# Kernel optimization log

Hardware: AMD Instinct MI355X
Metric: run time of the kernel (lower is better)

## Reference

```python
import jax, jax.numpy as jnp
import numpy as np

BSZ, MAX_LEN, INPUT_DIM = 4, 256, 1024
BIAFFINE, OUT, N_HEAD = 512, 512, 4
IN_HD = BIAFFINE // N_HEAD   # 128
OUT_HD = OUT // N_HEAD       # 128


def setup_inputs() -> dict:
    key = jax.random.key(0)
    ks = jax.random.split(key, 6)
    x = jax.random.normal(ks[0], (BSZ, MAX_LEN, INPUT_DIM), dtype=jnp.float32)
    # head/tail MLP linear params (dropout is identity at inference)
    scale_lin = 1.0 / np.sqrt(INPUT_DIM)
    Wh = jax.random.normal(ks[1], (BIAFFINE, INPUT_DIM), dtype=jnp.float32) * scale_lin
    bh = jnp.zeros((BIAFFINE,), dtype=jnp.float32)
    Wv = jax.random.normal(ks[2], (BIAFFINE, INPUT_DIM), dtype=jnp.float32) * scale_lin
    bv = jnp.zeros((BIAFFINE,), dtype=jnp.float32)
    # biaffine tensor, xavier_normal over last two dims fan
    xav = np.sqrt(2.0 / (IN_HD + IN_HD))
    W = jax.random.normal(ks[3], (N_HEAD, OUT_HD, IN_HD, IN_HD), dtype=jnp.float32) * xav
    return {"x": x, "Wh": Wh, "bh": bh, "Wv": Wv, "bv": bv, "W": W}


def reference(x, Wh, bh, Wv, bv, W):
    # head/tail MLPs: Linear + LeakyReLU (slope 0.01, torch default)
    h = jax.nn.leaky_relu(jnp.einsum('bld,od->blo', x, Wh) + bh)  # b l biaffine
    v = jax.nn.leaky_relu(jnp.einsum('bld,od->blo', x, Wv) + bv)
    bsz, max_len, _ = h.shape
    h = h.reshape(bsz, max_len, N_HEAD, IN_HD)
    v = v.reshape(bsz, max_len, N_HEAD, IN_HD)
    # 3-way biaffine contraction
    w = jnp.einsum('blhx,hdxy,bkhy->bhdlk', h, W, v)  # b h out_hd l k
    w = w.reshape(bsz, OUT, max_len, max_len)
    return jnp.transpose(w, (0, 2, 3, 1))  # b l k out
```

## Files before the change

### kernel.cpp

```cpp
#include <hip/hip_runtime.h>


typedef unsigned short u16;
typedef __attribute__((ext_vector_type(8))) short short8;
typedef __attribute__((ext_vector_type(4))) float f32x4;

typedef __attribute__((address_space(1))) const unsigned gu32;
typedef __attribute__((address_space(3))) unsigned lu32;

__device__ __forceinline__ u16 f2bf(float f) {
  union { float f; unsigned u; } c; c.f = f;
  unsigned u = c.u;
  return (u16)((u + 0x7FFFu + ((u >> 16) & 1u)) >> 16);
}

__device__ __forceinline__ unsigned pack2(float a, float b) {
  return ((unsigned)f2bf(b) << 16) | (unsigned)f2bf(a);
}

__device__ __forceinline__ uint4 pack8(const float* __restrict__ g) {
  float4 f0 = *(const float4*)(g);
  float4 f1 = *(const float4*)(g + 4);
  uint4 o;
  o.x = pack2(f0.x, f0.y);
  o.y = pack2(f0.z, f0.w);
  o.z = pack2(f1.x, f1.y);
  o.w = pack2(f1.z, f1.w);
  return o;
}

__device__ __forceinline__ void tile_compute(const u16* As, const u16* Bs,
                                             f32x4 acc[4][4], int wm, int wn,
                                             int frow, int kq) {
  short8 af[4], bfr[4];
#pragma unroll
  for (int i = 0; i < 4; ++i)
    af[i] = *(const short8*)(As + (size_t)(wm + i * 16 + frow) * 32 + kq);
#pragma unroll
  for (int j = 0; j < 4; ++j)
    bfr[j] = *(const short8*)(Bs + (size_t)(wn + j * 16 + frow) * 32 + kq);
#pragma unroll
  for (int i = 0; i < 4; ++i)
#pragma unroll
    for (int j = 0; j < 4; ++j)
      acc[i][j] = __builtin_amdgcn_mfma_f32_16x16x32_bf16(af[i], bfr[j], acc[i][j], 0, 0, 0);
}

__device__ __forceinline__ void stage_tile(const u16* __restrict__ g,
                                           u16* lds, int wave, int lane) {
#pragma unroll
  for (int t = 0; t < 8; ++t) {
    int qb = wave * 512 + t * 64;
    int q = qb + lane;
    const u16* src = g + (size_t)((q & 127) * 128 + (q >> 7) * 8);
    __builtin_amdgcn_global_load_lds((gu32*)src, (lu32*)(lds + (size_t)qb * 8),
                                     16, 0, 0);
  }
}

__device__ __forceinline__ void compute_fullK(const u16* As, const u16* Bs,
                                              f32x4 acc[4][4], int wm, int wn,
                                              int frow, int chi) {
#pragma unroll
  for (int ks = 0; ks < 4; ++ks) {
    int c = ks * 4 + chi;
    short8 af[4], bfr[4];
#pragma unroll
    for (int i = 0; i < 4; ++i)
      af[i] = *(const short8*)(As + ((size_t)c * 128 + wm + i * 16 + frow) * 8);
#pragma unroll
    for (int j = 0; j < 4; ++j)
      bfr[j] = *(const short8*)(Bs + ((size_t)c * 128 + wn + j * 16 + frow) * 8);
#pragma unroll
    for (int i = 0; i < 4; ++i)
#pragma unroll
      for (int j = 0; j < 4; ++j)
        acc[i][j] = __builtin_amdgcn_mfma_f32_16x16x32_bf16(af[i], bfr[j], acc[i][j], 0, 0, 0);
  }
}

__global__ __launch_bounds__(256) void k0_twp(const float* __restrict__ W,
                                              u16* __restrict__ Wb) {
  __shared__ u16 t[128][129];
  int slice = blockIdx.x;
  const float* src = W + (size_t)slice * 16384;
  u16* dst = Wb + (size_t)slice * 16384;
  int tid = threadIdx.x;
  for (int e = tid; e < 16384; e += 256) {
    int xi = e >> 7, yi = e & 127;
    t[xi][yi] = f2bf(src[e]);
  }
  __syncthreads();
  for (int e = tid; e < 16384; e += 256) {
    int yi = e >> 7, xi = e & 127;
    dst[e] = t[xi][yi];
  }
}

__global__ __launch_bounds__(256) void k1_mlp(const float* __restrict__ x,
                                              const float* __restrict__ Wh,
                                              const float* __restrict__ bh,
                                              const float* __restrict__ Wv,
                                              const float* __restrict__ bv,
                                              u16* __restrict__ hmat,
                                              u16* __restrict__ vmat) {
  __shared__ __align__(16) u16 As[128 * 32];
  __shared__ __align__(16) u16 Bs[128 * 32];
  int tid = threadIdx.x;
  int m0 = blockIdx.y * 128;
  int n0 = blockIdx.x * 128;
  bool isV = (n0 >= 512);
  const float* Wsel = isV ? Wv : Wh;
  const float* bsel = isV ? bv : bh;
  int nW = isV ? (n0 - 512) : n0;
  int wave = tid >> 6, lane = tid & 63;
  int wm = (wave & 1) * 64, wn = (wave >> 1) * 64;
  int r = tid >> 1, seg = tid & 1;
  int frow = lane & 15, kq = (lane >> 4) * 8;
  f32x4 acc[4][4];
  f32x4 z = {0.f, 0.f, 0.f, 0.f};
#pragma unroll
  for (int i = 0; i < 4; ++i)
#pragma unroll
    for (int j = 0; j < 4; ++j) acc[i][j] = z;

  for (int k0 = 0; k0 < 1024; k0 += 32) {
    const float* ga = x + (size_t)(m0 + r) * 1024 + k0 + seg * 16;
    const float* gb = Wsel + (size_t)(nW + r) * 1024 + k0 + seg * 16;
    uint4 a0 = pack8(ga), a1 = pack8(ga + 8);
    uint4 b0 = pack8(gb), b1 = pack8(gb + 8);
    __syncthreads();
    *(uint4*)(As + r * 32 + seg * 16) = a0;
    *(uint4*)(As + r * 32 + seg * 16 + 8) = a1;
    *(uint4*)(Bs + r * 32 + seg * 16) = b0;
    *(uint4*)(Bs + r * 32 + seg * 16 + 8) = b1;
    __syncthreads();
    tile_compute(As, Bs, acc, wm, wn, frow, kq);
  }

  u16* dst = isV ? vmat : hmat;
#pragma unroll
  for (int i = 0; i < 4; ++i)
#pragma unroll
    for (int j = 0; j < 4; ++j)
#pragma unroll
      for (int rg = 0; rg < 4; ++rg) {
        int ml = wm + i * 16 + (lane >> 4) * 4 + rg;
        int nl = wn + j * 16 + (lane & 15);
        int mg = m0 + ml;
        int ng = n0 + nl;
        float val = acc[i][j][rg] + bsel[nW + nl];
        val = (val >= 0.f) ? val : 0.01f * val;
        int bb = mg >> 8, ll = mg & 255;
        int head = (ng & 511) >> 7, xcol = ng & 127;
        dst[(((size_t)(bb * 4 + head)) * 256 + ll) * 128 + xcol] = f2bf(val);
      }
}

__global__ __launch_bounds__(256) void k2_uw(const u16* __restrict__ hmat,
                                             const u16* __restrict__ Wb,
                                             u16* __restrict__ u, int b0) {
  __shared__ __align__(16) u16 As[16384];
  __shared__ __align__(16) u16 Bs[16384];
  int tid = threadIdx.x, wave = tid >> 6, lane = tid & 63;
  int z = blockIdx.z;
  int b = b0 + (z >> 2), h = z & 3;
  int n0 = blockIdx.x * 128;
  int m0 = blockIdx.y * 128;
  const u16* A = hmat + ((size_t)(b * 4 + h) * 256 + m0) * 128;
  const u16* Bt = Wb + ((size_t)h * 16384 + n0) * 128;
  stage_tile(A, As, wave, lane);
  stage_tile(Bt, Bs, wave, lane);

  int wm = (wave & 1) * 64, wn = (wave >> 1) * 64;
  int frow = lane & 15, chi = lane >> 4;
  f32x4 acc[4][4];
  f32x4 zz = {0.f, 0.f, 0.f, 0.f};
#pragma unroll
  for (int i = 0; i < 4; ++i)
#pragma unroll
    for (int j = 0; j < 4; ++j) acc[i][j] = zz;

  __syncthreads();
  compute_fullK(As, Bs, acc, wm, wn, frow, chi);

  u16* C = u + ((size_t)z * 256 + m0) * 16384 + n0;
#pragma unroll
  for (int i = 0; i < 4; ++i)
#pragma unroll
    for (int j = 0; j < 4; ++j)
#pragma unroll
      for (int rg = 0; rg < 4; ++rg) {
        int ml = wm + i * 16 + (lane >> 4) * 4 + rg;
        int nl = wn + j * 16 + (lane & 15);
        C[(size_t)ml * 16384 + nl] = f2bf(acc[i][j][rg]);
      }
}

__global__ __launch_bounds__(256) void k3_out(const u16* __restrict__ vmat,
                                              const u16* __restrict__ u,
                                              float* __restrict__ out, int b0) {
  __shared__ __align__(16) u16 As[16384];
  __shared__ __align__(16) u16 Bs[16384];
  int tid = threadIdx.x, wave = tid >> 6, lane = tid & 63;
  int z = blockIdx.z;
  int b = b0 + (z >> 2), h = z & 3;
  int l = blockIdx.x;
  int k0t = blockIdx.y * 128;
  const u16* A = vmat + ((size_t)(b * 4 + h) * 256 + k0t) * 128;
  const u16* Bt = u + ((size_t)z * 256 + l) * 16384;
  stage_tile(A, As, wave, lane);
  stage_tile(Bt, Bs, wave, lane);

  int wm = (wave & 1) * 64, wn = (wave >> 1) * 64;
  int frow = lane & 15, chi = lane >> 4;
  f32x4 acc[4][4];
  f32x4 zz = {0.f, 0.f, 0.f, 0.f};
#pragma unroll
  for (int i = 0; i < 4; ++i)
#pragma unroll
    for (int j = 0; j < 4; ++j) acc[i][j] = zz;

  __syncthreads();
  compute_fullK(As, Bs, acc, wm, wn, frow, chi);

#pragma unroll
  for (int i = 0; i < 4; ++i)
#pragma unroll
    for (int j = 0; j < 4; ++j)
#pragma unroll
      for (int rg = 0; rg < 4; ++rg) {
        int kk = k0t + wm + i * 16 + (lane >> 4) * 4 + rg;
        int d = wn + j * 16 + (lane & 15);
        out[(((size_t)b * 256 + l) * 256 + kk) * 512 + h * 128 + d] = acc[i][j][rg];
      }
}

extern "C" void kernel_launch(void* const* d_in, const int* in_sizes, int n_in,
                              void* d_out, int out_size, void* d_ws, size_t ws_size,
                              hipStream_t stream) {
  const float* x = (const float*)d_in[0];
  const float* Wh = (const float*)d_in[1];
  const float* bh = (const float*)d_in[2];
  const float* Wv = (const float*)d_in[3];
  const float* bv = (const float*)d_in[4];
  const float* W = (const float*)d_in[5];
  float* out = (float*)d_out;

  char* ws = (char*)d_ws;
  u16* Wb = (u16*)(ws);
  u16* hmat = (u16*)(ws + (16u << 20));
  u16* vmat = (u16*)(ws + (17u << 20));
  u16* u = (u16*)(ws + (18u << 20));

  hipLaunchKernelGGL(k0_twp, dim3(512), dim3(256), 0, stream, W, Wb);
  hipLaunchKernelGGL(k1_mlp, dim3(8, 8), dim3(256), 0, stream, x, Wh, bh, Wv, bv,
                     hmat, vmat);

  size_t need = (18ull << 20) + (128ull << 20);
  if (ws_size >= need) {
    hipLaunchKernelGGL(k2_uw, dim3(128, 2, 16), dim3(256), 0, stream, hmat, Wb, u, 0);
    hipLaunchKernelGGL(k3_out, dim3(256, 2, 16), dim3(256), 0, stream, vmat, u, out, 0);
  } else {
    for (int b = 0; b < 4; ++b) {
      hipLaunchKernelGGL(k2_uw, dim3(128, 2, 4), dim3(256), 0, stream, hmat, Wb, u, b);
      hipLaunchKernelGGL(k3_out, dim3(256, 2, 4), dim3(256), 0, stream, vmat, u, out, b);
    }
  }
}
```

Measured before the change: 727.7 us.

## Pre-tile operands in chunked layout for contiguous LDS staging and XOR-swizzled u loads

The h/v projections and the transposed biaffine weight are now written in a k-chunked tile layout, so each 128x128 tile is one contiguous 32KB block. The block can then be staged into LDS with linear global_load_lds instead of the strided gather used before. The u operand in k3 is staged with an XOR swizzle on the chunk index, and the fragment reads apply the matching swizzle, which is meant to coalesce global reads of u rows and avoid LDS bank conflicts. The blockIdx.z mapping is reordered to put head outermost, which changes how blocks are grouped when they run.

```diff
diff --git a/kernel.cpp b/kernel.cpp
--- a/kernel.cpp
+++ b/kernel.cpp
@@ -29,38 +29,32 @@
   return o;
 }
 
-__device__ __forceinline__ void tile_compute(const u16* As, const u16* Bs,
-                                             f32x4 acc[4][4], int wm, int wn,
-                                             int frow, int kq) {
-  short8 af[4], bfr[4];
-#pragma unroll
-  for (int i = 0; i < 4; ++i)
-    af[i] = *(const short8*)(As + (size_t)(wm + i * 16 + frow) * 32 + kq);
-#pragma unroll
-  for (int j = 0; j < 4; ++j)
-    bfr[j] = *(const short8*)(Bs + (size_t)(wn + j * 16 + frow) * 32 + kq);
-#pragma unroll
-  for (int i = 0; i < 4; ++i)
-#pragma unroll
-    for (int j = 0; j < 4; ++j)
-      acc[i][j] = __builtin_amdgcn_mfma_f32_16x16x32_bf16(af[i], bfr[j], acc[i][j], 0, 0, 0);
-}
-
-__device__ __forceinline__ void stage_tile(const u16* __restrict__ g,
-                                           u16* lds, int wave, int lane) {
+__device__ __forceinline__ void stage_linear(const u16* __restrict__ g,
+                                             u16* lds, int wave, int lane) {
+#pragma unroll
+  for (int t = 0; t < 8; ++t) {
+    int qb = wave * 512 + t * 64;
+    __builtin_amdgcn_global_load_lds((gu32*)(g + (size_t)(qb + lane) * 8),
+                                     (lu32*)(lds + (size_t)qb * 8), 16, 0, 0);
+  }
+}
+
+__device__ __forceinline__ void stage_xor(const u16* __restrict__ g,
+                                          u16* lds, int wave, int lane) {
 #pragma unroll
   for (int t = 0; t < 8; ++t) {
     int qb = wave * 512 + t * 64;
     int q = qb + lane;
-    const u16* src = g + (size_t)((q & 127) * 128 + (q >> 7) * 8);
-    __builtin_amdgcn_global_load_lds((gu32*)src, (lu32*)(lds + (size_t)qb * 8),
-                                     16, 0, 0);
-  }
-}
-
-__device__ __forceinline__ void compute_fullK(const u16* As, const u16* Bs,
-                                              f32x4 acc[4][4], int wm, int wn,
-                                              int frow, int chi) {
+    int row = q >> 4, c = q & 15;
+    int su = row * 16 + (c ^ (row & 7));
+    __builtin_amdgcn_global_load_lds((gu32*)(g + (size_t)su * 8),
+                                     (lu32*)(lds + (size_t)qb * 8), 16, 0, 0);
+  }
+}
+
+__device__ __forceinline__ void compute_kk(const u16* As, const u16* Bs,
+                                           f32x4 acc[4][4], int wm, int wn,
+                                           int frow, int chi) {
 #pragma unroll
   for (int ks = 0; ks < 4; ++ks) {
     int c = ks * 4 + chi;
@@ -71,6 +65,29 @@
 #pragma unroll
     for (int j = 0; j < 4; ++j)
       bfr[j] = *(const short8*)(Bs + ((size_t)c * 128 + wn + j * 16 + frow) * 8);
+#pragma unroll
+    for (int i = 0; i < 4; ++i)
+#pragma unroll
+      for (int j = 0; j < 4; ++j)
+        acc[i][j] = __builtin_amdgcn_mfma_f32_16x16x32_bf16(af[i], bfr[j], acc[i][j], 0, 0, 0);
+  }
+}
+
+__device__ __forceinline__ void compute_kx(const u16* As, const u16* Bs,
+                                           f32x4 acc[4][4], int wm, int wn,
+                                           int frow, int chi) {
+#pragma unroll
+  for (int ks = 0; ks < 4; ++ks) {
+    int c = ks * 4 + chi;
+    short8 af[4], bfr[4];
+#pragma unroll
+    for (int i = 0; i < 4; ++i)
+      af[i] = *(const short8*)(As + ((size_t)c * 128 + wm + i * 16 + frow) * 8);
+#pragma unroll
+    for (int j = 0; j < 4; ++j) {
+      int rn = wn + j * 16 + frow;
+      bfr[j] = *(const short8*)(Bs + ((size_t)rn * 16 + (c ^ (rn & 7))) * 8);
+    }
 #pragma unroll
     for (int i = 0; i < 4; ++i)
 #pragma unroll
@@ -92,8 +109,8 @@
   }
   __syncthreads();
   for (int e = tid; e < 16384; e += 256) {
-    int yi = e >> 7, xi = e & 127;
-    dst[e] = t[xi][yi];
+    int c = e >> 10, rem = e & 1023, y = rem >> 3, xl = rem & 7;
+    dst[e] = t[c * 8 + xl][y];
   }
 }
 
@@ -135,7 +152,18 @@
     *(uint4*)(Bs + r * 32 + seg * 16) = b0;
     *(uint4*)(Bs + r * 32 + seg * 16 + 8) = b1;
     __syncthreads();
-    tile_compute(As, Bs, acc, wm, wn, frow, kq);
+    short8 af[4], bfr[4];
+#pragma unroll
+    for (int i = 0; i < 4; ++i)
+      af[i] = *(const short8*)(As + (size_t)(wm + i * 16 + frow) * 32 + kq);
+#pragma unroll
+    for (int j = 0; j < 4; ++j)
+      bfr[j] = *(const short8*)(Bs + (size_t)(wn + j * 16 + frow) * 32 + kq);
+#pragma unroll
+    for (int i = 0; i < 4; ++i)
+#pragma unroll
+      for (int j = 0; j < 4; ++j)
+        acc[i][j] = __builtin_amdgcn_mfma_f32_16x16x32_bf16(af[i], bfr[j], acc[i][j], 0, 0, 0);
   }
 
   u16* dst = isV ? vmat : hmat;
@@ -152,39 +180,42 @@
         float val = acc[i][j][rg] + bsel[nW + nl];
         val = (val >= 0.f) ? val : 0.01f * val;
         int bb = mg >> 8, ll = mg & 255;
-        int head = (ng & 511) >> 7, xcol = ng & 127;
-        dst[(((size_t)(bb * 4 + head)) * 256 + ll) * 128 + xcol] = f2bf(val);
+        int head = (ng & 511) >> 7, xc = ng & 127;
+        int zi = head * 4 + bb;
+        dst[((size_t)zi * 2 + (ll >> 7)) * 16384 + (xc >> 3) * 1024 +
+            (ll & 127) * 8 + (xc & 7)] = f2bf(val);
       }
 }
 
 __global__ __launch_bounds__(256) void k2_uw(const u16* __restrict__ hmat,
                                              const u16* __restrict__ Wb,
-                                             u16* __restrict__ u, int b0) {
+                                             u16* __restrict__ u, int b0, int nz) {
   __shared__ __align__(16) u16 As[16384];
   __shared__ __align__(16) u16 Bs[16384];
   int tid = threadIdx.x, wave = tid >> 6, lane = tid & 63;
-  int z = blockIdx.z;
-  int b = b0 + (z >> 2), h = z & 3;
-  int n0 = blockIdx.x * 128;
+  int zz = blockIdx.z;
+  int h, b;
+  if (nz == 16) { h = zz >> 2; b = zz & 3; } else { h = zz; b = b0; }
+  int zi_hm = h * 4 + b;
+  int zi_u = zz;
+  int d = blockIdx.x;
   int m0 = blockIdx.y * 128;
-  const u16* A = hmat + ((size_t)(b * 4 + h) * 256 + m0) * 128;
-  const u16* Bt = Wb + ((size_t)h * 16384 + n0) * 128;
-  stage_tile(A, As, wave, lane);
-  stage_tile(Bt, Bs, wave, lane);
+  stage_linear(hmat + ((size_t)zi_hm * 2 + (m0 >> 7)) * 16384, As, wave, lane);
+  stage_linear(Wb + ((size_t)h * 128 + d) * 16384, Bs, wave, lane);
 
   int wm = (wave & 1) * 64, wn = (wave >> 1) * 64;
   int frow = lane & 15, chi = lane >> 4;
   f32x4 acc[4][4];
-  f32x4 zz = {0.f, 0.f, 0.f, 0.f};
-#pragma unroll
-  for (int i = 0; i < 4; ++i)
-#pragma unroll
-    for (int j = 0; j < 4; ++j) acc[i][j] = zz;
+  f32x4 zz4 = {0.f, 0.f, 0.f, 0.f};
+#pragma unroll
+  for (int i = 0; i < 4; ++i)
+#pragma unroll
+    for (int j = 0; j < 4; ++j) acc[i][j] = zz4;
 
   __syncthreads();
-  compute_fullK(As, Bs, acc, wm, wn, frow, chi);
-
-  u16* C = u + ((size_t)z * 256 + m0) * 16384 + n0;
+  compute_kk(As, Bs, acc, wm, wn, frow, chi);
+
+  u16* C = u + ((size_t)zi_u * 256 + m0) * 16384 + (d << 7);
 #pragma unroll
   for (int i = 0; i < 4; ++i)
 #pragma unroll
@@ -199,30 +230,31 @@
 
 __global__ __launch_bounds__(256) void k3_out(const u16* __restrict__ vmat,
                                               const u16* __restrict__ u,
-                                              float* __restrict__ out, int b0) {
+                                              float* __restrict__ out, int b0, int nz) {
   __shared__ __align__(16) u16 As[16384];
   __shared__ __align__(16) u16 Bs[16384];
   int tid = threadIdx.x, wave = tid >> 6, lane = tid & 63;
-  int z = blockIdx.z;
-  int b = b0 + (z >> 2), h = z & 3;
+  int zz = blockIdx.z;
+  int h, b;
+  if (nz == 16) { h = zz >> 2; b = zz & 3; } else { h = zz; b = b0; }
+  int zi_vm = h * 4 + b;
+  int zi_u = zz;
   int l = blockIdx.x;
   int k0t = blockIdx.y * 128;
-  const u16* A = vmat + ((size_t)(b * 4 + h) * 256 + k0t) * 128;
-  const u16* Bt = u + ((size_t)z * 256 + l) * 16384;
-  stage_tile(A, As, wave, lane);
-  stage_tile(Bt, Bs, wave, lane);
+  stage_linear(vmat + ((size_t)zi_vm * 2 + (k0t >> 7)) * 16384, As, wave, lane);
+  stage_xor(u + ((size_t)zi_u * 256 + l) * 16384, Bs, wave, lane);
 
   int wm = (wave & 1) * 64, wn = (wave >> 1) * 64;
   int frow = lane & 15, chi = lane >> 4;
   f32x4 acc[4][4];
-  f32x4 zz = {0.f, 0.f, 0.f, 0.f};
-#pragma unroll
-  for (int i = 0; i < 4; ++i)
-#pragma unroll
-    for (int j = 0; j < 4; ++j) acc[i][j] = zz;
+  f32x4 zz4 = {0.f, 0.f, 0.f, 0.f};
+#pragma unroll
+  for (int i = 0; i < 4; ++i)
+#pragma unroll
+    for (int j = 0; j < 4; ++j) acc[i][j] = zz4;
 
   __syncthreads();
-  compute_fullK(As, Bs, acc, wm, wn, frow, chi);
+  compute_kx(As, Bs, acc, wm, wn, frow, chi);
 
 #pragma unroll
   for (int i = 0; i < 4; ++i)
@@ -231,8 +263,8 @@
 #pragma unroll
       for (int rg = 0; rg < 4; ++rg) {
         int kk = k0t + wm + i * 16 + (lane >> 4) * 4 + rg;
-        int d = wn + j * 16 + (lane & 15);
-        out[(((size_t)b * 256 + l) * 256 + kk) * 512 + h * 128 + d] = acc[i][j][rg];
+        int dd = wn + j * 16 + (lane & 15);
+        out[(((size_t)b * 256 + l) * 256 + kk) * 512 + h * 128 + dd] = acc[i][j][rg];
       }
 }
 
@@ -259,12 +291,12 @@
 
   size_t need = (18ull << 20) + (128ull << 20);
   if (ws_size >= need) {
-    hipLaunchKernelGGL(k2_uw, dim3(128, 2, 16), dim3(256), 0, stream, hmat, Wb, u, 0);
-    hipLaunchKernelGGL(k3_out, dim3(256, 2, 16), dim3(256), 0, stream, vmat, u, out, 0);
+    hipLaunchKernelGGL(k2_uw, dim3(128, 2, 16), dim3(256), 0, stream, hmat, Wb, u, 0, 16);
+    hipLaunchKernelGGL(k3_out, dim3(256, 2, 16), dim3(256), 0, stream, vmat, u, out, 0, 16);
   } else {
     for (int b = 0; b < 4; ++b) {
-      hipLaunchKernelGGL(k2_uw, dim3(128, 2, 4), dim3(256), 0, stream, hmat, Wb, u, b);
-      hipLaunchKernelGGL(k3_out, dim3(256, 2, 4), dim3(256), 0, stream, vmat, u, out, b);
+      hipLaunchKernelGGL(k2_uw, dim3(128, 2, 4), dim3(256), 0, stream, hmat, Wb, u, b, 4);
+      hipLaunchKernelGGL(k3_out, dim3(256, 2, 4), dim3(256), 0, stream, vmat, u, out, b, 4);
     }
   }
 }
```

Measured after the change: 678.1 us. -6.8%, faster.
